# Kernel tuning notes

Measured on AMD Instinct MI355X. Metric: run time of the kernel, lower is better.

Reference implementation:

```python
import jax, jax.numpy as jnp
import numpy as np

B, N, M, D = 4096, 50, 64, 64   # batch, fields_dim, embedding_dim, product_layer_dim
V = 100000                      # features_dim (vocab)
HIDDEN = [512, 256, 128]
BN_EPS = 1e-3


def setup_inputs() -> dict:
    key = jax.random.key(0)
    ks = jax.random.split(key, 32)
    inp = {
        "feature_value": jax.random.uniform(ks[0], (B, N), dtype=jnp.float32),
        "embedding_index": jax.random.randint(ks[1], (B, N), 0, V, dtype=jnp.int32),
        "emb_table": jax.random.uniform(ks[2], (V, M), dtype=jnp.float32, minval=-0.05, maxval=0.05),
        "linear_signals": jax.random.normal(ks[3], (D, N, M), dtype=jnp.float32) * 0.05,
        "theta": jax.random.normal(ks[4], (D, N), dtype=jnp.float32) * 0.05,
        "quad_w": jax.random.normal(ks[5], (D, M, M), dtype=jnp.float32) * 0.05,
    }
    in_dim = 3 * D  # concat(l_z, l_p_inner, l_p_outer)
    dims = [in_dim] + HIDDEN
    k = 6
    for i, (di, do) in enumerate(zip(dims[:-1], dims[1:])):
        inp[f"W{i}"] = jax.random.normal(ks[k], (di, do), dtype=jnp.float32) * (1.0 / np.sqrt(di)); k += 1
        inp[f"b{i}"] = jnp.zeros((do,), dtype=jnp.float32)
        inp[f"g{i}"] = jnp.ones((do,), dtype=jnp.float32)
        inp[f"be{i}"] = jnp.zeros((do,), dtype=jnp.float32)
        inp[f"m{i}"] = jnp.zeros((do,), dtype=jnp.float32)
        inp[f"v{i}"] = jnp.ones((do,), dtype=jnp.float32)
    inp["Wout"] = jax.random.normal(ks[k], (HIDDEN[-1], 1), dtype=jnp.float32) * (1.0 / np.sqrt(HIDDEN[-1]))
    inp["bout"] = jnp.zeros((1,), dtype=jnp.float32)
    return inp


def _pnn_forward(feature_value, embedding_index, emb_table, linear_signals, theta, quad_w,
                 dense_params, Wout, bout):
    # features: [b, n, m] = embedding lookup scaled per-field by feature_value
    feats = emb_table[embedding_index] * feature_value[:, :, None]
    # linear signal: 'bnm,dnm->bd'
    l_z = jnp.einsum('bnm,dnm->bd', feats, linear_signals)
    # ipnn branch: delta = 'dn,bnm->bdnm'; l_p = sum delta*delta over (n,m)
    # algebraic rewrite (same math): sum_n theta_dn^2 * (sum_m feats_bnm^2)
    l_p_in = jnp.einsum('bn,dn->bd', jnp.sum(feats * feats, axis=2), theta * theta)
    # opnn branch: p = outer(sum_feats, sum_feats); 'bmn,dmn->bd'
    s = jnp.sum(feats, axis=1)  # [b, m]
    l_p_out = jnp.einsum('bm,dmn,bn->bd', s, quad_w, s)
    x = jnp.concatenate([l_z, l_p_in, l_p_out], axis=1)  # [b, 3d]
    # MLP stack: Dense -> BatchNorm(inference) -> ReLU (dropout is identity at eval)
    for (W, b, g, be, mu, var) in dense_params:
        x = x @ W + b
        x = g * (x - mu) * jax.lax.rsqrt(var + BN_EPS) + be
        x = jax.nn.relu(x)
    return jax.nn.sigmoid(x @ Wout + bout)


def reference(feature_value, embedding_index, emb_table, linear_signals, theta, quad_w,
              W0, b0, g0, be0, m0, v0,
              W1, b1, g1, be1, m1, v1,
              W2, b2, g2, be2, m2, v2,
              Wout, bout):
    dense_params = [(W0, b0, g0, be0, m0, v0),
                    (W1, b1, g1, be1, m1, v1),
                    (W2, b2, g2, be2, m2, v2)]
    return _pnn_forward(feature_value, embedding_index, emb_table, linear_signals, theta,
                        quad_w, dense_params, Wout, bout)
```

## Files before the change

### kernel.cpp

```cpp
#include <hip/hip_runtime.h>
#include <hip/hip_bf16.h>
#include <math.h>

#define B 4096
#define NF 50
#define BN_EPS 1e-3f
#define ROWS 16

typedef float f32x4 __attribute__((ext_vector_type(4)));
typedef __bf16 bf16x8 __attribute__((ext_vector_type(8)));
#define MFMA __builtin_amdgcn_mfma_f32_16x16x32_bf16

__device__ __forceinline__ unsigned short f2b(float x) {
  unsigned u = __float_as_uint(x);
  return (unsigned short)((u + 0x7FFFu + ((u >> 16) & 1u)) >> 16);
}
__device__ __forceinline__ unsigned packbf(float a, float b) {
  return ((unsigned)f2b(b) << 16) | (unsigned)f2b(a);
}
__device__ __forceinline__ float bs2f(unsigned short u) {
  return __uint_as_float(((unsigned)u) << 16);
}

#define WS_LS  0
#define WS_QW  204800
#define WS_W0  466944
#define WS_W1  565248
#define WS_W2  696320

__global__ __launch_bounds__(256) void prep(
    const float* __restrict__ ls, const float* __restrict__ qw,
    const float* __restrict__ W0, const float* __restrict__ W1,
    const float* __restrict__ W2, unsigned short* __restrict__ ws)
{
  int bid = blockIdx.x, t = threadIdx.x;
  if (bid < 228) {
    int o = (bid * 256 + t) * 8;
    const float* src = (o < 204800) ? (ls + o) : (qw + (o - 204800));
    float4 a = *(const float4*)src, b = *(const float4*)(src + 4);
    int4 v = {(int)packbf(a.x, a.y), (int)packbf(a.z, a.w),
              (int)packbf(b.x, b.y), (int)packbf(b.z, b.w)};
    *(int4*)&ws[o] = v;
    return;
  }
  __shared__ unsigned short sh[64 * 72];
  int id = bid - 228;
  const float* W; int K, Ncols, kt, nt, wofs;
  if (id < 24)      { W = W0; K = 192; Ncols = 512; kt = id >> 3; nt = id & 7;  wofs = WS_W0; }
  else if (id < 56) { int j = id - 24; W = W1; K = 512; Ncols = 256; kt = j >> 2; nt = j & 3; wofs = WS_W1; }
  else              { int j = id - 56; W = W2; K = 256; Ncols = 128; kt = j >> 1; nt = j & 1; wofs = WS_W2; }
  int k0 = kt * 64, n0 = nt * 64;
  {
    int r = t >> 2, cs = (t & 3) * 16;
    const float* src = W + (size_t)(k0 + r) * Ncols + n0 + cs;
    float4 a = *(const float4*)src, b = *(const float4*)(src + 4);
    float4 c = *(const float4*)(src + 8), d = *(const float4*)(src + 12);
    unsigned short* dst = &sh[r * 72 + cs];
    *(int4*)dst = int4{(int)packbf(a.x, a.y), (int)packbf(a.z, a.w),
                       (int)packbf(b.x, b.y), (int)packbf(b.z, b.w)};
    *(int4*)(dst + 8) = int4{(int)packbf(c.x, c.y), (int)packbf(c.z, c.w),
                             (int)packbf(d.x, d.y), (int)packbf(d.z, d.w)};
  }
  __syncthreads();
  {
    int nr = t >> 2, ks = (t & 3) * 16;
    unsigned short vbuf[16];
#pragma unroll
    for (int j = 0; j < 16; ++j) vbuf[j] = sh[(ks + j) * 72 + nr];
    unsigned short* dst = &ws[wofs + (size_t)(n0 + nr) * K + k0 + ks];
    *(int4*)dst = *(int4*)&vbuf[0];
    *(int4*)(dst + 8) = *(int4*)&vbuf[8];
  }
}

__global__ __launch_bounds__(512) void pnn_main(
    const float* __restrict__ fv, const int* __restrict__ idx,
    const float* __restrict__ emb, const float* __restrict__ theta,
    const unsigned short* __restrict__ ws,
    const float* __restrict__ b0p, const float* __restrict__ g0p,
    const float* __restrict__ be0p, const float* __restrict__ m0p,
    const float* __restrict__ v0p,
    const float* __restrict__ b1p, const float* __restrict__ g1p,
    const float* __restrict__ be1p, const float* __restrict__ m1p,
    const float* __restrict__ v1p,
    const float* __restrict__ b2p, const float* __restrict__ g2p,
    const float* __restrict__ be2p, const float* __restrict__ m2p,
    const float* __restrict__ v2p,
    const float* __restrict__ Wout, const float* __restrict__ boutp,
    float* __restrict__ out)
{
  __shared__ unsigned short feats[25 * 16 * 136];
  __shared__ int   idx_s[ROWS * NF];
  __shared__ float fv_s[ROWS * NF];
  __shared__ float s_s[ROWS * 68];
  __shared__ float sq_s[ROWS * 64];
  __shared__ unsigned short x_s[ROWS * 200];

  unsigned short* h0_s = feats;
  unsigned short* h1_s = feats + 8320;
  unsigned short* h2_s = feats + 12544;

  const unsigned short* lsb = ws + WS_LS;
  const unsigned short* qwb = ws + WS_QW;
  const unsigned short* w0t = ws + WS_W0;
  const unsigned short* w1t = ws + WS_W1;
  const unsigned short* w2t = ws + WS_W2;

  const int t    = threadIdx.x;
  const int w    = t >> 6;
  const int l    = t & 63;
  const int m16  = l & 15;
  const int qoff = (l >> 4) * 8;
  const int b0   = blockIdx.x * ROWS;

  for (int i = t; i < ROWS * NF; i += 512) {
    idx_s[i] = idx[b0 * NF + i];
    fv_s[i]  = fv[b0 * NF + i];
  }
  __syncthreads();

  {
    const int row = t >> 5;
    const int m2  = (t & 31) * 2;
    float s0 = 0.f, s1 = 0.f;
#pragma unroll 5
    for (int c = 0; c < 25; ++c) {
      int n0 = 2 * c, n1 = n0 + 1;
      int iv0 = idx_s[row * NF + n0], iv1 = idx_s[row * NF + n1];
      float f0 = fv_s[row * NF + n0], f1 = fv_s[row * NF + n1];
      float2 e0 = *(const float2*)(emb + (size_t)iv0 * 64 + m2);
      float2 e1 = *(const float2*)(emb + (size_t)iv1 * 64 + m2);
      float p00 = f0 * e0.x, p01 = f0 * e0.y;
      float p10 = f1 * e1.x, p11 = f1 * e1.y;
      unsigned short* fc = feats + c * 2176 + row * 136;
      *(unsigned*)&fc[m2]      = packbf(p00, p01);
      *(unsigned*)&fc[64 + m2] = packbf(p10, p11);
      s0 += p00 + p10; s1 += p01 + p11;
      float q0 = p00 * p00 + p01 * p01;
      float q1 = p10 * p10 + p11 * p11;
      q0 += __shfl_xor(q0, 16); q0 += __shfl_xor(q0, 8); q0 += __shfl_xor(q0, 4);
      q0 += __shfl_xor(q0, 2);  q0 += __shfl_xor(q0, 1);
      q1 += __shfl_xor(q1, 16); q1 += __shfl_xor(q1, 8); q1 += __shfl_xor(q1, 4);
      q1 += __shfl_xor(q1, 2);  q1 += __shfl_xor(q1, 1);
      if ((t & 31) == 0) { sq_s[row * 64 + n0] = q0; sq_s[row * 64 + n1] = q1; }
    }
    float2 sv; sv.x = s0; sv.y = s1;
    *(float2*)&s_s[row * 68 + m2] = sv;
  }
  __syncthreads();

  if (w < 4) {
    const int dt = w;
    f32x4 a0v = {0.f, 0.f, 0.f, 0.f}, a1v = {0.f, 0.f, 0.f, 0.f};
    const unsigned short* lp0 = lsb + (size_t)(dt * 16 + m16) * 3200 + qoff;
    for (int c = 0; c < 25; ++c) {
      const unsigned short* fc = feats + c * 2176 + m16 * 136 + qoff;
      const unsigned short* lp = lp0 + c * 128;
#pragma unroll
      for (int s = 0; s < 4; ++s) {
        bf16x8 av = *(const bf16x8*)(fc + s * 32);
        bf16x8 bv = *(const bf16x8*)(lp + s * 32);
        if (s & 1) a1v = MFMA(av, bv, a1v, 0, 0, 0);
        else       a0v = MFMA(av, bv, a0v, 0, 0, 0);
      }
    }
#pragma unroll
    for (int r = 0; r < 4; ++r)
      x_s[((l >> 4) * 4 + r) * 200 + dt * 16 + m16] = f2b(a0v[r] + a1v[r]);
    {
      int d = dt * 16 + m16;
      float acc[4] = {0.f, 0.f, 0.f, 0.f};
      for (int n = 0; n < NF; ++n) {
        float th = theta[d * NF + n];
        float th2 = th * th;
#pragma unroll
        for (int r = 0; r < 4; ++r)
          acc[r] += sq_s[((l >> 4) * 4 + r) * 64 + n] * th2;
      }
#pragma unroll
      for (int r = 0; r < 4; ++r)
        x_s[((l >> 4) * 4 + r) * 200 + 64 + d] = f2b(acc[r]);
    }
  } else {
    const int dt = w - 4;
    const int row = m16;
    const int nb = qoff;
    float sn[16];
    *(float4*)&sn[0]  = *(const float4*)&s_s[row * 68 + nb];
    *(float4*)&sn[4]  = *(const float4*)&s_s[row * 68 + nb + 4];
    *(float4*)&sn[8]  = *(const float4*)&s_s[row * 68 + 32 + nb];
    *(float4*)&sn[12] = *(const float4*)&s_s[row * 68 + 32 + nb + 4];
    f32x4 a0v = {0.f, 0.f, 0.f, 0.f}, a1v = {0.f, 0.f, 0.f, 0.f};
    const unsigned short* qp0 = qwb + (size_t)(dt * 16 + m16) * 4096 + qoff;
    for (int m = 0; m < 64; ++m) {
      float sm = s_s[row * 68 + m];
      union { unsigned u[4]; bf16x8 v; } af0, af1;
#pragma unroll
      for (int j = 0; j < 4; ++j) {
        af0.u[j] = packbf(sm * sn[2 * j],     sm * sn[2 * j + 1]);
        af1.u[j] = packbf(sm * sn[8 + 2 * j], sm * sn[8 + 2 * j + 1]);
      }
      const unsigned short* qp = qp0 + m * 64;
      bf16x8 b0v = *(const bf16x8*)qp;
      bf16x8 b1v = *(const bf16x8*)(qp + 32);
      a0v = MFMA(af0.v, b0v, a0v, 0, 0, 0);
      a1v = MFMA(af1.v, b1v, a1v, 0, 0, 0);
    }
#pragma unroll
    for (int r = 0; r < 4; ++r)
      x_s[((l >> 4) * 4 + r) * 200 + 128 + dt * 16 + m16] = f2b(a0v[r] + a1v[r]);
  }
  __syncthreads();

  {
    int ar = m16 * 200 + qoff;
    bf16x8 xa[6];
#pragma unroll
    for (int kc = 0; kc < 6; ++kc) xa[kc] = *(const bf16x8*)&x_s[ar + kc * 32];
    for (int j = 0; j < 4; ++j) {
      int n0 = (w * 4 + j) * 16;
      const unsigned short* wp = w0t + (size_t)(n0 + m16) * 192 + qoff;
      f32x4 ha = {0.f, 0.f, 0.f, 0.f}, hb = {0.f, 0.f, 0.f, 0.f};
#pragma unroll
      for (int kc = 0; kc < 6; ++kc) {
        bf16x8 bv = *(const bf16x8*)(wp + kc * 32);
        if (kc & 1) hb = MFMA(xa[kc], bv, hb, 0, 0, 0);
        else        ha = MFMA(xa[kc], bv, ha, 0, 0, 0);
      }
      int n = n0 + m16;
      float sc = g0p[n] * rsqrtf(v0p[n] + BN_EPS);
      float sh = be0p[n] + (b0p[n] - m0p[n]) * sc;
#pragma unroll
      for (int r = 0; r < 4; ++r) {
        float v = fmaxf((ha[r] + hb[r]) * sc + sh, 0.f);
        h0_s[((l >> 4) * 4 + r) * 520 + n] = f2b(v);
      }
    }
  }
  __syncthreads();

  for (int j = 0; j < 2; ++j) {
    int n0 = (w * 2 + j) * 16;
    const unsigned short* wp = w1t + (size_t)(n0 + m16) * 512 + qoff;
    int ar = m16 * 520 + qoff;
    f32x4 ha = {0.f, 0.f, 0.f, 0.f}, hb = {0.f, 0.f, 0.f, 0.f};
#pragma unroll
    for (int kc = 0; kc < 16; ++kc) {
      bf16x8 av = *(const bf16x8*)&h0_s[ar + kc * 32];
      bf16x8 bv = *(const bf16x8*)(wp + kc * 32);
      if (kc & 1) hb = MFMA(av, bv, hb, 0, 0, 0);
      else        ha = MFMA(av, bv, ha, 0, 0, 0);
    }
    int n = n0 + m16;
    float sc = g1p[n] * rsqrtf(v1p[n] + BN_EPS);
    float sh = be1p[n] + (b1p[n] - m1p[n]) * sc;
#pragma unroll
    for (int r = 0; r < 4; ++r) {
      float v = fmaxf((ha[r] + hb[r]) * sc + sh, 0.f);
      h1_s[((l >> 4) * 4 + r) * 264 + n] = f2b(v);
    }
  }
  __syncthreads();

  {
    int n0 = w * 16;
    const unsigned short* wp = w2t + (size_t)(n0 + m16) * 256 + qoff;
    int ar = m16 * 264 + qoff;
    f32x4 ha = {0.f, 0.f, 0.f, 0.f}, hb = {0.f, 0.f, 0.f, 0.f};
#pragma unroll
    for (int kc = 0; kc < 8; ++kc) {
      bf16x8 av = *(const bf16x8*)&h1_s[ar + kc * 32];
      bf16x8 bv = *(const bf16x8*)(wp + kc * 32);
      if (kc & 1) hb = MFMA(av, bv, hb, 0, 0, 0);
      else        ha = MFMA(av, bv, ha, 0, 0, 0);
    }
    int n = n0 + m16;
    float sc = g2p[n] * rsqrtf(v2p[n] + BN_EPS);
    float sh = be2p[n] + (b2p[n] - m2p[n]) * sc;
#pragma unroll
    for (int r = 0; r < 4; ++r) {
      float v = fmaxf((ha[r] + hb[r]) * sc + sh, 0.f);
      h2_s[((l >> 4) * 4 + r) * 136 + n] = f2b(v);
    }
  }
  __syncthreads();

  if (t < 128) {
    int bb = t >> 3, seg = t & 7;
    float a = 0.f;
#pragma unroll
    for (int j = 0; j < 16; ++j) {
      int k = seg * 16 + j;
      a += bs2f(h2_s[bb * 136 + k]) * Wout[k];
    }
    a += __shfl_xor(a, 4); a += __shfl_xor(a, 2); a += __shfl_xor(a, 1);
    if (seg == 0) out[b0 + bb] = 1.f / (1.f + expf(-(a + boutp[0])));
  }
}

extern "C" void kernel_launch(void* const* d_in, const int* in_sizes, int n_in,
                              void* d_out, int out_size, void* d_ws, size_t ws_size,
                              hipStream_t stream)
{
  (void)in_sizes; (void)n_in; (void)out_size; (void)ws_size;
  unsigned short* ws = (unsigned short*)d_ws;

  prep<<<292, 256, 0, stream>>>(
      (const float*)d_in[3], (const float*)d_in[5], (const float*)d_in[6],
      (const float*)d_in[12], (const float*)d_in[18], ws);

  pnn_main<<<B / ROWS, 512, 0, stream>>>(
      (const float*)d_in[0], (const int*)d_in[1], (const float*)d_in[2],
      (const float*)d_in[4], ws,
      (const float*)d_in[7],  (const float*)d_in[8],  (const float*)d_in[9],
      (const float*)d_in[10], (const float*)d_in[11],
      (const float*)d_in[13], (const float*)d_in[14], (const float*)d_in[15],
      (const float*)d_in[16], (const float*)d_in[17],
      (const float*)d_in[19], (const float*)d_in[20], (const float*)d_in[21],
      (const float*)d_in[22], (const float*)d_in[23],
      (const float*)d_in[24], (const float*)d_in[25],
      (float*)d_out);
}
```

Baseline: 182.2 us.

## Drop weight prep kernel and convert fp32 weights to bf16 inside main kernel

Removes the separate prep launch that pre-converted linear_signals, quad_w and the MLP weights to bf16, with the MLP weights also transposed. The main kernel now reads the fp32 weights directly and packs them to bf16 in registers, using strided scalar loads for the untransposed MLP weights. This saves one launch and the workspace round trip. In exchange, each of the 256 blocks re-reads twice the weight bytes and does its own conversion, and the MLP weight reads become strided, uncoalesced scalar loads.

```diff
diff --git a/kernel.cpp b/kernel.cpp
--- a/kernel.cpp
+++ b/kernel.cpp
@@ -21,71 +21,36 @@
 __device__ __forceinline__ float bs2f(unsigned short u) {
   return __uint_as_float(((unsigned)u) << 16);
 }
-
-#define WS_LS  0
-#define WS_QW  204800
-#define WS_W0  466944
-#define WS_W1  565248
-#define WS_W2  696320
-
-__global__ __launch_bounds__(256) void prep(
-    const float* __restrict__ ls, const float* __restrict__ qw,
-    const float* __restrict__ W0, const float* __restrict__ W1,
-    const float* __restrict__ W2, unsigned short* __restrict__ ws)
-{
-  int bid = blockIdx.x, t = threadIdx.x;
-  if (bid < 228) {
-    int o = (bid * 256 + t) * 8;
-    const float* src = (o < 204800) ? (ls + o) : (qw + (o - 204800));
-    float4 a = *(const float4*)src, b = *(const float4*)(src + 4);
-    int4 v = {(int)packbf(a.x, a.y), (int)packbf(a.z, a.w),
-              (int)packbf(b.x, b.y), (int)packbf(b.z, b.w)};
-    *(int4*)&ws[o] = v;
-    return;
-  }
-  __shared__ unsigned short sh[64 * 72];
-  int id = bid - 228;
-  const float* W; int K, Ncols, kt, nt, wofs;
-  if (id < 24)      { W = W0; K = 192; Ncols = 512; kt = id >> 3; nt = id & 7;  wofs = WS_W0; }
-  else if (id < 56) { int j = id - 24; W = W1; K = 512; Ncols = 256; kt = j >> 2; nt = j & 3; wofs = WS_W1; }
-  else              { int j = id - 56; W = W2; K = 256; Ncols = 128; kt = j >> 1; nt = j & 1; wofs = WS_W2; }
-  int k0 = kt * 64, n0 = nt * 64;
-  {
-    int r = t >> 2, cs = (t & 3) * 16;
-    const float* src = W + (size_t)(k0 + r) * Ncols + n0 + cs;
-    float4 a = *(const float4*)src, b = *(const float4*)(src + 4);
-    float4 c = *(const float4*)(src + 8), d = *(const float4*)(src + 12);
-    unsigned short* dst = &sh[r * 72 + cs];
-    *(int4*)dst = int4{(int)packbf(a.x, a.y), (int)packbf(a.z, a.w),
-                       (int)packbf(b.x, b.y), (int)packbf(b.z, b.w)};
-    *(int4*)(dst + 8) = int4{(int)packbf(c.x, c.y), (int)packbf(c.z, c.w),
-                             (int)packbf(d.x, d.y), (int)packbf(d.z, d.w)};
-  }
-  __syncthreads();
-  {
-    int nr = t >> 2, ks = (t & 3) * 16;
-    unsigned short vbuf[16];
-#pragma unroll
-    for (int j = 0; j < 16; ++j) vbuf[j] = sh[(ks + j) * 72 + nr];
-    unsigned short* dst = &ws[wofs + (size_t)(n0 + nr) * K + k0 + ks];
-    *(int4*)dst = *(int4*)&vbuf[0];
-    *(int4*)(dst + 8) = *(int4*)&vbuf[8];
-  }
-}
-
-__global__ __launch_bounds__(512) void pnn_main(
+__device__ __forceinline__ bf16x8 ld_bf8(const float* p) {
+  float4 a = *(const float4*)p, b = *(const float4*)(p + 4);
+  union { unsigned u[4]; bf16x8 v; } r;
+  r.u[0] = packbf(a.x, a.y); r.u[1] = packbf(a.z, a.w);
+  r.u[2] = packbf(b.x, b.y); r.u[3] = packbf(b.z, b.w);
+  return r.v;
+}
+__device__ __forceinline__ bf16x8 ld_bf8_strided(const float* p, int stride) {
+  float f[8];
+#pragma unroll
+  for (int j = 0; j < 8; ++j) f[j] = p[j * stride];
+  union { unsigned u[4]; bf16x8 v; } r;
+  r.u[0] = packbf(f[0], f[1]); r.u[1] = packbf(f[2], f[3]);
+  r.u[2] = packbf(f[4], f[5]); r.u[3] = packbf(f[6], f[7]);
+  return r.v;
+}
+
+__global__ __launch_bounds__(512) void pnn_all(
     const float* __restrict__ fv, const int* __restrict__ idx,
     const float* __restrict__ emb, const float* __restrict__ theta,
-    const unsigned short* __restrict__ ws,
-    const float* __restrict__ b0p, const float* __restrict__ g0p,
-    const float* __restrict__ be0p, const float* __restrict__ m0p,
-    const float* __restrict__ v0p,
-    const float* __restrict__ b1p, const float* __restrict__ g1p,
-    const float* __restrict__ be1p, const float* __restrict__ m1p,
-    const float* __restrict__ v1p,
-    const float* __restrict__ b2p, const float* __restrict__ g2p,
-    const float* __restrict__ be2p, const float* __restrict__ m2p,
-    const float* __restrict__ v2p,
+    const float* __restrict__ ls, const float* __restrict__ qw,
+    const float* __restrict__ W0, const float* __restrict__ b0p,
+    const float* __restrict__ g0p, const float* __restrict__ be0p,
+    const float* __restrict__ m0p, const float* __restrict__ v0p,
+    const float* __restrict__ W1, const float* __restrict__ b1p,
+    const float* __restrict__ g1p, const float* __restrict__ be1p,
+    const float* __restrict__ m1p, const float* __restrict__ v1p,
+    const float* __restrict__ W2, const float* __restrict__ b2p,
+    const float* __restrict__ g2p, const float* __restrict__ be2p,
+    const float* __restrict__ m2p, const float* __restrict__ v2p,
     const float* __restrict__ Wout, const float* __restrict__ boutp,
     float* __restrict__ out)
 {
@@ -99,12 +64,6 @@
   unsigned short* h0_s = feats;
   unsigned short* h1_s = feats + 8320;
   unsigned short* h2_s = feats + 12544;
-
-  const unsigned short* lsb = ws + WS_LS;
-  const unsigned short* qwb = ws + WS_QW;
-  const unsigned short* w0t = ws + WS_W0;
-  const unsigned short* w1t = ws + WS_W1;
-  const unsigned short* w2t = ws + WS_W2;
 
   const int t    = threadIdx.x;
   const int w    = t >> 6;
@@ -152,14 +111,14 @@
   if (w < 4) {
     const int dt = w;
     f32x4 a0v = {0.f, 0.f, 0.f, 0.f}, a1v = {0.f, 0.f, 0.f, 0.f};
-    const unsigned short* lp0 = lsb + (size_t)(dt * 16 + m16) * 3200 + qoff;
+    const float* lp0 = ls + (size_t)(dt * 16 + m16) * 3200 + qoff;
     for (int c = 0; c < 25; ++c) {
       const unsigned short* fc = feats + c * 2176 + m16 * 136 + qoff;
-      const unsigned short* lp = lp0 + c * 128;
+      const float* lp = lp0 + c * 128;
 #pragma unroll
       for (int s = 0; s < 4; ++s) {
         bf16x8 av = *(const bf16x8*)(fc + s * 32);
-        bf16x8 bv = *(const bf16x8*)(lp + s * 32);
+        bf16x8 bv = ld_bf8(lp + s * 32);
         if (s & 1) a1v = MFMA(av, bv, a1v, 0, 0, 0);
         else       a0v = MFMA(av, bv, a0v, 0, 0, 0);
       }
@@ -191,7 +150,7 @@
     *(float4*)&sn[8]  = *(const float4*)&s_s[row * 68 + 32 + nb];
     *(float4*)&sn[12] = *(const float4*)&s_s[row * 68 + 32 + nb + 4];
     f32x4 a0v = {0.f, 0.f, 0.f, 0.f}, a1v = {0.f, 0.f, 0.f, 0.f};
-    const unsigned short* qp0 = qwb + (size_t)(dt * 16 + m16) * 4096 + qoff;
+    const float* qp0 = qw + (size_t)(dt * 16 + m16) * 4096 + qoff;
     for (int m = 0; m < 64; ++m) {
       float sm = s_s[row * 68 + m];
       union { unsigned u[4]; bf16x8 v; } af0, af1;
@@ -200,9 +159,9 @@
         af0.u[j] = packbf(sm * sn[2 * j],     sm * sn[2 * j + 1]);
         af1.u[j] = packbf(sm * sn[8 + 2 * j], sm * sn[8 + 2 * j + 1]);
       }
-      const unsigned short* qp = qp0 + m * 64;
-      bf16x8 b0v = *(const bf16x8*)qp;
-      bf16x8 b1v = *(const bf16x8*)(qp + 32);
+      const float* qp = qp0 + m * 64;
+      bf16x8 b0v = ld_bf8(qp);
+      bf16x8 b1v = ld_bf8(qp + 32);
       a0v = MFMA(af0.v, b0v, a0v, 0, 0, 0);
       a1v = MFMA(af1.v, b1v, a1v, 0, 0, 0);
     }
@@ -219,11 +178,10 @@
     for (int kc = 0; kc < 6; ++kc) xa[kc] = *(const bf16x8*)&x_s[ar + kc * 32];
     for (int j = 0; j < 4; ++j) {
       int n0 = (w * 4 + j) * 16;
-      const unsigned short* wp = w0t + (size_t)(n0 + m16) * 192 + qoff;
       f32x4 ha = {0.f, 0.f, 0.f, 0.f}, hb = {0.f, 0.f, 0.f, 0.f};
 #pragma unroll
       for (int kc = 0; kc < 6; ++kc) {
-        bf16x8 bv = *(const bf16x8*)(wp + kc * 32);
+        bf16x8 bv = ld_bf8_strided(W0 + (size_t)(kc * 32 + qoff) * 512 + n0 + m16, 512);
         if (kc & 1) hb = MFMA(xa[kc], bv, hb, 0, 0, 0);
         else        ha = MFMA(xa[kc], bv, ha, 0, 0, 0);
       }
@@ -241,13 +199,12 @@
 
   for (int j = 0; j < 2; ++j) {
     int n0 = (w * 2 + j) * 16;
-    const unsigned short* wp = w1t + (size_t)(n0 + m16) * 512 + qoff;
     int ar = m16 * 520 + qoff;
     f32x4 ha = {0.f, 0.f, 0.f, 0.f}, hb = {0.f, 0.f, 0.f, 0.f};
 #pragma unroll
     for (int kc = 0; kc < 16; ++kc) {
       bf16x8 av = *(const bf16x8*)&h0_s[ar + kc * 32];
-      bf16x8 bv = *(const bf16x8*)(wp + kc * 32);
+      bf16x8 bv = ld_bf8_strided(W1 + (size_t)(kc * 32 + qoff) * 256 + n0 + m16, 256);
       if (kc & 1) hb = MFMA(av, bv, hb, 0, 0, 0);
       else        ha = MFMA(av, bv, ha, 0, 0, 0);
     }
@@ -264,13 +221,12 @@
 
   {
     int n0 = w * 16;
-    const unsigned short* wp = w2t + (size_t)(n0 + m16) * 256 + qoff;
     int ar = m16 * 264 + qoff;
     f32x4 ha = {0.f, 0.f, 0.f, 0.f}, hb = {0.f, 0.f, 0.f, 0.f};
 #pragma unroll
     for (int kc = 0; kc < 8; ++kc) {
       bf16x8 av = *(const bf16x8*)&h1_s[ar + kc * 32];
-      bf16x8 bv = *(const bf16x8*)(wp + kc * 32);
+      bf16x8 bv = ld_bf8_strided(W2 + (size_t)(kc * 32 + qoff) * 128 + n0 + m16, 128);
       if (kc & 1) hb = MFMA(av, bv, hb, 0, 0, 0);
       else        ha = MFMA(av, bv, ha, 0, 0, 0);
     }
@@ -302,22 +258,17 @@
                               void* d_out, int out_size, void* d_ws, size_t ws_size,
                               hipStream_t stream)
 {
-  (void)in_sizes; (void)n_in; (void)out_size; (void)ws_size;
-  unsigned short* ws = (unsigned short*)d_ws;
-
-  prep<<<292, 256, 0, stream>>>(
-      (const float*)d_in[3], (const float*)d_in[5], (const float*)d_in[6],
-      (const float*)d_in[12], (const float*)d_in[18], ws);
-
-  pnn_main<<<B / ROWS, 512, 0, stream>>>(
+  (void)in_sizes; (void)n_in; (void)out_size; (void)d_ws; (void)ws_size;
+
+  pnn_all<<<B / ROWS, 512, 0, stream>>>(
       (const float*)d_in[0], (const int*)d_in[1], (const float*)d_in[2],
-      (const float*)d_in[4], ws,
-      (const float*)d_in[7],  (const float*)d_in[8],  (const float*)d_in[9],
-      (const float*)d_in[10], (const float*)d_in[11],
-      (const float*)d_in[13], (const float*)d_in[14], (const float*)d_in[15],
-      (const float*)d_in[16], (const float*)d_in[17],
-      (const float*)d_in[19], (const float*)d_in[20], (const float*)d_in[21],
-      (const float*)d_in[22], (const float*)d_in[23],
+      (const float*)d_in[4], (const float*)d_in[3], (const float*)d_in[5],
+      (const float*)d_in[6],  (const float*)d_in[7],  (const float*)d_in[8],
+      (const float*)d_in[9],  (const float*)d_in[10], (const float*)d_in[11],
+      (const float*)d_in[12], (const float*)d_in[13], (const float*)d_in[14],
+      (const float*)d_in[15], (const float*)d_in[16], (const float*)d_in[17],
+      (const float*)d_in[18], (const float*)d_in[19], (const float*)d_in[20],
+      (const float*)d_in[21], (const float*)d_in[22], (const float*)d_in[23],
       (const float*)d_in[24], (const float*)d_in[25],
       (float*)d_out);
 }
```

Result: slower. 245.0 us (+34.4%).

## Halve rows per block to 8 and remap gather, MFMA rows and theta staging

Applied to the files above, without the earlier changes.

Cuts the rows per block from 16 to 8, which doubles the grid to 512 blocks and shrinks shared memory. The launch-bounds minimum of 4 blocks per SM is meant to raise occupancy. The embedding gather is remapped to one wave per row with coalesced scalar loads, and theta squared is staged in shared memory instead of being re-read from global. MFMA tiles still compute 16 rows, so half the matrix work is duplicated and half the lanes are masked on stores, and every block now reloads all weights.

```diff
diff --git a/kernel.cpp b/kernel.cpp
--- a/kernel.cpp
+++ b/kernel.cpp
@@ -5,7 +5,7 @@
 #define B 4096
 #define NF 50
 #define BN_EPS 1e-3f
-#define ROWS 16
+#define ROWS 8
 
 typedef float f32x4 __attribute__((ext_vector_type(4)));
 typedef __bf16 bf16x8 __attribute__((ext_vector_type(8)));
@@ -73,7 +73,7 @@
   }
 }
 
-__global__ __launch_bounds__(512) void pnn_main(
+__global__ __launch_bounds__(512, 4) void pnn_main(
     const float* __restrict__ fv, const int* __restrict__ idx,
     const float* __restrict__ emb, const float* __restrict__ theta,
     const unsigned short* __restrict__ ws,
@@ -89,16 +89,17 @@
     const float* __restrict__ Wout, const float* __restrict__ boutp,
     float* __restrict__ out)
 {
-  __shared__ unsigned short feats[25 * 16 * 136];
+  __shared__ unsigned short feats[25 * ROWS * 136];
   __shared__ int   idx_s[ROWS * NF];
   __shared__ float fv_s[ROWS * NF];
+  __shared__ float th2_s[64 * NF];
   __shared__ float s_s[ROWS * 68];
   __shared__ float sq_s[ROWS * 64];
   __shared__ unsigned short x_s[ROWS * 200];
 
   unsigned short* h0_s = feats;
-  unsigned short* h1_s = feats + 8320;
-  unsigned short* h2_s = feats + 12544;
+  unsigned short* h1_s = feats + 4160;
+  unsigned short* h2_s = feats + 6272;
 
   const unsigned short* lsb = ws + WS_LS;
   const unsigned short* qwb = ws + WS_QW;
@@ -117,35 +118,24 @@
     idx_s[i] = idx[b0 * NF + i];
     fv_s[i]  = fv[b0 * NF + i];
   }
-  __syncthreads();
-
-  {
-    const int row = t >> 5;
-    const int m2  = (t & 31) * 2;
-    float s0 = 0.f, s1 = 0.f;
-#pragma unroll 5
-    for (int c = 0; c < 25; ++c) {
-      int n0 = 2 * c, n1 = n0 + 1;
-      int iv0 = idx_s[row * NF + n0], iv1 = idx_s[row * NF + n1];
-      float f0 = fv_s[row * NF + n0], f1 = fv_s[row * NF + n1];
-      float2 e0 = *(const float2*)(emb + (size_t)iv0 * 64 + m2);
-      float2 e1 = *(const float2*)(emb + (size_t)iv1 * 64 + m2);
-      float p00 = f0 * e0.x, p01 = f0 * e0.y;
-      float p10 = f1 * e1.x, p11 = f1 * e1.y;
-      unsigned short* fc = feats + c * 2176 + row * 136;
-      *(unsigned*)&fc[m2]      = packbf(p00, p01);
-      *(unsigned*)&fc[64 + m2] = packbf(p10, p11);
-      s0 += p00 + p10; s1 += p01 + p11;
-      float q0 = p00 * p00 + p01 * p01;
-      float q1 = p10 * p10 + p11 * p11;
-      q0 += __shfl_xor(q0, 16); q0 += __shfl_xor(q0, 8); q0 += __shfl_xor(q0, 4);
-      q0 += __shfl_xor(q0, 2);  q0 += __shfl_xor(q0, 1);
-      q1 += __shfl_xor(q1, 16); q1 += __shfl_xor(q1, 8); q1 += __shfl_xor(q1, 4);
-      q1 += __shfl_xor(q1, 2);  q1 += __shfl_xor(q1, 1);
-      if ((t & 31) == 0) { sq_s[row * 64 + n0] = q0; sq_s[row * 64 + n1] = q1; }
-    }
-    float2 sv; sv.x = s0; sv.y = s1;
-    *(float2*)&s_s[row * 68 + m2] = sv;
+  for (int i = t; i < 64 * NF; i += 512) { float v = theta[i]; th2_s[i] = v * v; }
+  __syncthreads();
+
+  {
+    float s0 = 0.f;
+#pragma unroll 2
+    for (int n = 0; n < NF; ++n) {
+      int iv = idx_s[w * NF + n];
+      float fvv = fv_s[w * NF + n];
+      float p = fvv * emb[(size_t)iv * 64 + l];
+      feats[(n >> 1) * (ROWS * 136) + w * 136 + (n & 1) * 64 + l] = f2b(p);
+      s0 += p;
+      float q = p * p;
+      q += __shfl_xor(q, 32); q += __shfl_xor(q, 16); q += __shfl_xor(q, 8);
+      q += __shfl_xor(q, 4);  q += __shfl_xor(q, 2);  q += __shfl_xor(q, 1);
+      if (l == 0) sq_s[w * 64 + n] = q;
+    }
+    s_s[w * 68 + l] = s0;
   }
   __syncthreads();
 
@@ -153,8 +143,9 @@
     const int dt = w;
     f32x4 a0v = {0.f, 0.f, 0.f, 0.f}, a1v = {0.f, 0.f, 0.f, 0.f};
     const unsigned short* lp0 = lsb + (size_t)(dt * 16 + m16) * 3200 + qoff;
+    const int arow = (m16 & 7) * 136 + qoff;
     for (int c = 0; c < 25; ++c) {
-      const unsigned short* fc = feats + c * 2176 + m16 * 136 + qoff;
+      const unsigned short* fc = feats + c * (ROWS * 136) + arow;
       const unsigned short* lp = lp0 + c * 128;
 #pragma unroll
       for (int s = 0; s < 4; ++s) {
@@ -164,15 +155,16 @@
         else       a0v = MFMA(av, bv, a0v, 0, 0, 0);
       }
     }
-#pragma unroll
-    for (int r = 0; r < 4; ++r)
-      x_s[((l >> 4) * 4 + r) * 200 + dt * 16 + m16] = f2b(a0v[r] + a1v[r]);
-    {
+    if (l < 32) {
+#pragma unroll
+      for (int r = 0; r < 4; ++r)
+        x_s[((l >> 4) * 4 + r) * 200 + dt * 16 + m16] = f2b(a0v[r] + a1v[r]);
+    }
+    if (l < 32) {
       int d = dt * 16 + m16;
       float acc[4] = {0.f, 0.f, 0.f, 0.f};
       for (int n = 0; n < NF; ++n) {
-        float th = theta[d * NF + n];
-        float th2 = th * th;
+        float th2 = th2_s[d * NF + n];
 #pragma unroll
         for (int r = 0; r < 4; ++r)
           acc[r] += sq_s[((l >> 4) * 4 + r) * 64 + n] * th2;
@@ -183,7 +175,7 @@
     }
   } else {
     const int dt = w - 4;
-    const int row = m16;
+    const int row = m16 & 7;
     const int nb = qoff;
     float sn[16];
     *(float4*)&sn[0]  = *(const float4*)&s_s[row * 68 + nb];
@@ -206,14 +198,16 @@
       a0v = MFMA(af0.v, b0v, a0v, 0, 0, 0);
       a1v = MFMA(af1.v, b1v, a1v, 0, 0, 0);
     }
-#pragma unroll
-    for (int r = 0; r < 4; ++r)
-      x_s[((l >> 4) * 4 + r) * 200 + 128 + dt * 16 + m16] = f2b(a0v[r] + a1v[r]);
-  }
-  __syncthreads();
-
-  {
-    int ar = m16 * 200 + qoff;
+    if (l < 32) {
+#pragma unroll
+      for (int r = 0; r < 4; ++r)
+        x_s[((l >> 4) * 4 + r) * 200 + 128 + dt * 16 + m16] = f2b(a0v[r] + a1v[r]);
+    }
+  }
+  __syncthreads();
+
+  {
+    int ar = (m16 & 7) * 200 + qoff;
     bf16x8 xa[6];
 #pragma unroll
     for (int kc = 0; kc < 6; ++kc) xa[kc] = *(const bf16x8*)&x_s[ar + kc * 32];
@@ -227,13 +221,15 @@
         if (kc & 1) hb = MFMA(xa[kc], bv, hb, 0, 0, 0);
         else        ha = MFMA(xa[kc], bv, ha, 0, 0, 0);
       }
-      int n = n0 + m16;
-      float sc = g0p[n] * rsqrtf(v0p[n] + BN_EPS);
-      float sh = be0p[n] + (b0p[n] - m0p[n]) * sc;
-#pragma unroll
-      for (int r = 0; r < 4; ++r) {
-        float v = fmaxf((ha[r] + hb[r]) * sc + sh, 0.f);
-        h0_s[((l >> 4) * 4 + r) * 520 + n] = f2b(v);
+      if (l < 32) {
+        int n = n0 + m16;
+        float sc = g0p[n] * rsqrtf(v0p[n] + BN_EPS);
+        float sh = be0p[n] + (b0p[n] - m0p[n]) * sc;
+#pragma unroll
+        for (int r = 0; r < 4; ++r) {
+          float v = fmaxf((ha[r] + hb[r]) * sc + sh, 0.f);
+          h0_s[((l >> 4) * 4 + r) * 520 + n] = f2b(v);
+        }
       }
     }
   }
@@ -242,7 +238,7 @@
   for (int j = 0; j < 2; ++j) {
     int n0 = (w * 2 + j) * 16;
     const unsigned short* wp = w1t + (size_t)(n0 + m16) * 512 + qoff;
-    int ar = m16 * 520 + qoff;
+    int ar = (m16 & 7) * 520 + qoff;
     f32x4 ha = {0.f, 0.f, 0.f, 0.f}, hb = {0.f, 0.f, 0.f, 0.f};
 #pragma unroll
     for (int kc = 0; kc < 16; ++kc) {
@@ -251,13 +247,15 @@
       if (kc & 1) hb = MFMA(av, bv, hb, 0, 0, 0);
       else        ha = MFMA(av, bv, ha, 0, 0, 0);
     }
-    int n = n0 + m16;
-    float sc = g1p[n] * rsqrtf(v1p[n] + BN_EPS);
-    float sh = be1p[n] + (b1p[n] - m1p[n]) * sc;
-#pragma unroll
-    for (int r = 0; r < 4; ++r) {
-      float v = fmaxf((ha[r] + hb[r]) * sc + sh, 0.f);
-      h1_s[((l >> 4) * 4 + r) * 264 + n] = f2b(v);
+    if (l < 32) {
+      int n = n0 + m16;
+      float sc = g1p[n] * rsqrtf(v1p[n] + BN_EPS);
+      float sh = be1p[n] + (b1p[n] - m1p[n]) * sc;
+#pragma unroll
+      for (int r = 0; r < 4; ++r) {
+        float v = fmaxf((ha[r] + hb[r]) * sc + sh, 0.f);
+        h1_s[((l >> 4) * 4 + r) * 264 + n] = f2b(v);
+      }
     }
   }
   __syncthreads();
@@ -265,7 +263,7 @@
   {
     int n0 = w * 16;
     const unsigned short* wp = w2t + (size_t)(n0 + m16) * 256 + qoff;
-    int ar = m16 * 264 + qoff;
+    int ar = (m16 & 7) * 264 + qoff;
     f32x4 ha = {0.f, 0.f, 0.f, 0.f}, hb = {0.f, 0.f, 0.f, 0.f};
 #pragma unroll
     for (int kc = 0; kc < 8; ++kc) {
@@ -274,18 +272,20 @@
       if (kc & 1) hb = MFMA(av, bv, hb, 0, 0, 0);
       else        ha = MFMA(av, bv, ha, 0, 0, 0);
     }
-    int n = n0 + m16;
-    float sc = g2p[n] * rsqrtf(v2p[n] + BN_EPS);
-    float sh = be2p[n] + (b2p[n] - m2p[n]) * sc;
-#pragma unroll
-    for (int r = 0; r < 4; ++r) {
-      float v = fmaxf((ha[r] + hb[r]) * sc + sh, 0.f);
-      h2_s[((l >> 4) * 4 + r) * 136 + n] = f2b(v);
-    }
-  }
-  __syncthreads();
-
-  if (t < 128) {
+    if (l < 32) {
+      int n = n0 + m16;
+      float sc = g2p[n] * rsqrtf(v2p[n] + BN_EPS);
+      float sh = be2p[n] + (b2p[n] - m2p[n]) * sc;
+#pragma unroll
+      for (int r = 0; r < 4; ++r) {
+        float v = fmaxf((ha[r] + hb[r]) * sc + sh, 0.f);
+        h2_s[((l >> 4) * 4 + r) * 136 + n] = f2b(v);
+      }
+    }
+  }
+  __syncthreads();
+
+  if (t < 64) {
     int bb = t >> 3, seg = t & 7;
     float a = 0.f;
 #pragma unroll
```

Result: slower. 228.6 us (+25.4%).

## Batch global loads ahead of MFMA chains and cache squared theta in LDS

Applied to the files above, without the earlier changes.

Restructures the embedding gather, linear-signal, quadratic and MLP loops so that groups of global loads (embedding rows, bf16 weight fragments) are issued into register arrays before the dependent MFMA or arithmetic runs. The goal is more memory-level parallelism and better hiding of global-load latency. It also precomputes theta squared into shared memory once per block, so the ipnn loop no longer does per-lane global loads and squares. The cost is higher register pressure, which may lower occupancy, plus extra LDS and a per-block theta load.

```diff
diff --git a/kernel.cpp b/kernel.cpp
--- a/kernel.cpp
+++ b/kernel.cpp
@@ -92,6 +92,7 @@
   __shared__ unsigned short feats[25 * 16 * 136];
   __shared__ int   idx_s[ROWS * NF];
   __shared__ float fv_s[ROWS * NF];
+  __shared__ float th2_s[64 * NF];
   __shared__ float s_s[ROWS * 68];
   __shared__ float sq_s[ROWS * 64];
   __shared__ unsigned short x_s[ROWS * 200];
@@ -117,32 +118,41 @@
     idx_s[i] = idx[b0 * NF + i];
     fv_s[i]  = fv[b0 * NF + i];
   }
+  for (int i = t; i < 64 * NF; i += 512) { float v = theta[i]; th2_s[i] = v * v; }
   __syncthreads();
 
   {
     const int row = t >> 5;
     const int m2  = (t & 31) * 2;
     float s0 = 0.f, s1 = 0.f;
-#pragma unroll 5
-    for (int c = 0; c < 25; ++c) {
-      int n0 = 2 * c, n1 = n0 + 1;
-      int iv0 = idx_s[row * NF + n0], iv1 = idx_s[row * NF + n1];
-      float f0 = fv_s[row * NF + n0], f1 = fv_s[row * NF + n1];
-      float2 e0 = *(const float2*)(emb + (size_t)iv0 * 64 + m2);
-      float2 e1 = *(const float2*)(emb + (size_t)iv1 * 64 + m2);
-      float p00 = f0 * e0.x, p01 = f0 * e0.y;
-      float p10 = f1 * e1.x, p11 = f1 * e1.y;
-      unsigned short* fc = feats + c * 2176 + row * 136;
-      *(unsigned*)&fc[m2]      = packbf(p00, p01);
-      *(unsigned*)&fc[64 + m2] = packbf(p10, p11);
-      s0 += p00 + p10; s1 += p01 + p11;
-      float q0 = p00 * p00 + p01 * p01;
-      float q1 = p10 * p10 + p11 * p11;
-      q0 += __shfl_xor(q0, 16); q0 += __shfl_xor(q0, 8); q0 += __shfl_xor(q0, 4);
-      q0 += __shfl_xor(q0, 2);  q0 += __shfl_xor(q0, 1);
-      q1 += __shfl_xor(q1, 16); q1 += __shfl_xor(q1, 8); q1 += __shfl_xor(q1, 4);
-      q1 += __shfl_xor(q1, 2);  q1 += __shfl_xor(q1, 1);
-      if ((t & 31) == 0) { sq_s[row * 64 + n0] = q0; sq_s[row * 64 + n1] = q1; }
+    for (int g = 0; g < 5; ++g) {
+      float2 e[10];
+#pragma unroll
+      for (int j = 0; j < 5; ++j) {
+        int n0 = (g * 5 + j) * 2;
+        int iv0 = idx_s[row * NF + n0], iv1 = idx_s[row * NF + n0 + 1];
+        e[2 * j]     = *(const float2*)(emb + (size_t)iv0 * 64 + m2);
+        e[2 * j + 1] = *(const float2*)(emb + (size_t)iv1 * 64 + m2);
+      }
+#pragma unroll
+      for (int j = 0; j < 5; ++j) {
+        int c = g * 5 + j;
+        int n0 = 2 * c, n1 = n0 + 1;
+        float f0 = fv_s[row * NF + n0], f1 = fv_s[row * NF + n1];
+        float p00 = f0 * e[2 * j].x,     p01 = f0 * e[2 * j].y;
+        float p10 = f1 * e[2 * j + 1].x, p11 = f1 * e[2 * j + 1].y;
+        unsigned short* fc = feats + c * 2176 + row * 136;
+        *(unsigned*)&fc[m2]      = packbf(p00, p01);
+        *(unsigned*)&fc[64 + m2] = packbf(p10, p11);
+        s0 += p00 + p10; s1 += p01 + p11;
+        float q0 = p00 * p00 + p01 * p01;
+        float q1 = p10 * p10 + p11 * p11;
+        q0 += __shfl_xor(q0, 16); q0 += __shfl_xor(q0, 8); q0 += __shfl_xor(q0, 4);
+        q0 += __shfl_xor(q0, 2);  q0 += __shfl_xor(q0, 1);
+        q1 += __shfl_xor(q1, 16); q1 += __shfl_xor(q1, 8); q1 += __shfl_xor(q1, 4);
+        q1 += __shfl_xor(q1, 2);  q1 += __shfl_xor(q1, 1);
+        if ((t & 31) == 0) { sq_s[row * 64 + n0] = q0; sq_s[row * 64 + n1] = q1; }
+      }
     }
     float2 sv; sv.x = s0; sv.y = s1;
     *(float2*)&s_s[row * 68 + m2] = sv;
@@ -153,15 +163,25 @@
     const int dt = w;
     f32x4 a0v = {0.f, 0.f, 0.f, 0.f}, a1v = {0.f, 0.f, 0.f, 0.f};
     const unsigned short* lp0 = lsb + (size_t)(dt * 16 + m16) * 3200 + qoff;
-    for (int c = 0; c < 25; ++c) {
-      const unsigned short* fc = feats + c * 2176 + m16 * 136 + qoff;
-      const unsigned short* lp = lp0 + c * 128;
-#pragma unroll
-      for (int s = 0; s < 4; ++s) {
-        bf16x8 av = *(const bf16x8*)(fc + s * 32);
-        bf16x8 bv = *(const bf16x8*)(lp + s * 32);
-        if (s & 1) a1v = MFMA(av, bv, a1v, 0, 0, 0);
-        else       a0v = MFMA(av, bv, a0v, 0, 0, 0);
+    const int arow = m16 * 136 + qoff;
+    for (int g = 0; g < 5; ++g) {
+      bf16x8 bv[20];
+#pragma unroll
+      for (int cc = 0; cc < 5; ++cc) {
+        const unsigned short* lp = lp0 + (g * 5 + cc) * 128;
+#pragma unroll
+        for (int s4 = 0; s4 < 4; ++s4)
+          bv[cc * 4 + s4] = *(const bf16x8*)(lp + s4 * 32);
+      }
+#pragma unroll
+      for (int cc = 0; cc < 5; ++cc) {
+        const unsigned short* fc = feats + (g * 5 + cc) * 2176 + arow;
+#pragma unroll
+        for (int s4 = 0; s4 < 4; ++s4) {
+          bf16x8 av = *(const bf16x8*)(fc + s4 * 32);
+          if (s4 & 1) a1v = MFMA(av, bv[cc * 4 + s4], a1v, 0, 0, 0);
+          else        a0v = MFMA(av, bv[cc * 4 + s4], a0v, 0, 0, 0);
+        }
       }
     }
 #pragma unroll
@@ -171,8 +191,7 @@
       int d = dt * 16 + m16;
       float acc[4] = {0.f, 0.f, 0.f, 0.f};
       for (int n = 0; n < NF; ++n) {
-        float th = theta[d * NF + n];
-        float th2 = th * th;
+        float th2 = th2_s[d * NF + n];
 #pragma unroll
         for (int r = 0; r < 4; ++r)
           acc[r] += sq_s[((l >> 4) * 4 + r) * 64 + n] * th2;
@@ -192,19 +211,26 @@
     *(float4*)&sn[12] = *(const float4*)&s_s[row * 68 + 32 + nb + 4];
     f32x4 a0v = {0.f, 0.f, 0.f, 0.f}, a1v = {0.f, 0.f, 0.f, 0.f};
     const unsigned short* qp0 = qwb + (size_t)(dt * 16 + m16) * 4096 + qoff;
-    for (int m = 0; m < 64; ++m) {
-      float sm = s_s[row * 68 + m];
-      union { unsigned u[4]; bf16x8 v; } af0, af1;
-#pragma unroll
-      for (int j = 0; j < 4; ++j) {
-        af0.u[j] = packbf(sm * sn[2 * j],     sm * sn[2 * j + 1]);
-        af1.u[j] = packbf(sm * sn[8 + 2 * j], sm * sn[8 + 2 * j + 1]);
-      }
-      const unsigned short* qp = qp0 + m * 64;
-      bf16x8 b0v = *(const bf16x8*)qp;
-      bf16x8 b1v = *(const bf16x8*)(qp + 32);
-      a0v = MFMA(af0.v, b0v, a0v, 0, 0, 0);
-      a1v = MFMA(af1.v, b1v, a1v, 0, 0, 0);
+    for (int g = 0; g < 8; ++g) {
+      bf16x8 bv[16];
+#pragma unroll
+      for (int mi = 0; mi < 8; ++mi) {
+        const unsigned short* qp = qp0 + (g * 8 + mi) * 64;
+        bv[2 * mi]     = *(const bf16x8*)qp;
+        bv[2 * mi + 1] = *(const bf16x8*)(qp + 32);
+      }
+#pragma unroll
+      for (int mi = 0; mi < 8; ++mi) {
+        float sm = s_s[row * 68 + g * 8 + mi];
+        union { unsigned u[4]; bf16x8 v; } af0, af1;
+#pragma unroll
+        for (int j = 0; j < 4; ++j) {
+          af0.u[j] = packbf(sm * sn[2 * j],     sm * sn[2 * j + 1]);
+          af1.u[j] = packbf(sm * sn[8 + 2 * j], sm * sn[8 + 2 * j + 1]);
+        }
+        a0v = MFMA(af0.v, bv[2 * mi],     a0v, 0, 0, 0);
+        a1v = MFMA(af1.v, bv[2 * mi + 1], a1v, 0, 0, 0);
+      }
     }
 #pragma unroll
     for (int r = 0; r < 4; ++r)
@@ -220,12 +246,14 @@
     for (int j = 0; j < 4; ++j) {
       int n0 = (w * 4 + j) * 16;
       const unsigned short* wp = w0t + (size_t)(n0 + m16) * 192 + qoff;
+      bf16x8 bv[6];
+#pragma unroll
+      for (int kc = 0; kc < 6; ++kc) bv[kc] = *(const bf16x8*)(wp + kc * 32);
       f32x4 ha = {0.f, 0.f, 0.f, 0.f}, hb = {0.f, 0.f, 0.f, 0.f};
 #pragma unroll
       for (int kc = 0; kc < 6; ++kc) {
-        bf16x8 bv = *(const bf16x8*)(wp + kc * 32);
-        if (kc & 1) hb = MFMA(xa[kc], bv, hb, 0, 0, 0);
-        else        ha = MFMA(xa[kc], bv, ha, 0, 0, 0);
+        if (kc & 1) hb = MFMA(xa[kc], bv[kc], hb, 0, 0, 0);
+        else        ha = MFMA(xa[kc], bv[kc], ha, 0, 0, 0);
       }
       int n = n0 + m16;
       float sc = g0p[n] * rsqrtf(v0p[n] + BN_EPS);
@@ -242,14 +270,16 @@
   for (int j = 0; j < 2; ++j) {
     int n0 = (w * 2 + j) * 16;
     const unsigned short* wp = w1t + (size_t)(n0 + m16) * 512 + qoff;
+    bf16x8 bv[16];
+#pragma unroll
+    for (int kc = 0; kc < 16; ++kc) bv[kc] = *(const bf16x8*)(wp + kc * 32);
     int ar = m16 * 520 + qoff;
     f32x4 ha = {0.f, 0.f, 0.f, 0.f}, hb = {0.f, 0.f, 0.f, 0.f};
 #pragma unroll
     for (int kc = 0; kc < 16; ++kc) {
       bf16x8 av = *(const bf16x8*)&h0_s[ar + kc * 32];
-      bf16x8 bv = *(const bf16x8*)(wp + kc * 32);
-      if (kc & 1) hb = MFMA(av, bv, hb, 0, 0, 0);
-      else        ha = MFMA(av, bv, ha, 0, 0, 0);
+      if (kc & 1) hb = MFMA(av, bv[kc], hb, 0, 0, 0);
+      else        ha = MFMA(av, bv[kc], ha, 0, 0, 0);
     }
     int n = n0 + m16;
     float sc = g1p[n] * rsqrtf(v1p[n] + BN_EPS);
@@ -265,14 +295,16 @@
   {
     int n0 = w * 16;
     const unsigned short* wp = w2t + (size_t)(n0 + m16) * 256 + qoff;
+    bf16x8 bv[8];
+#pragma unroll
+    for (int kc = 0; kc < 8; ++kc) bv[kc] = *(const bf16x8*)(wp + kc * 32);
     int ar = m16 * 264 + qoff;
     f32x4 ha = {0.f, 0.f, 0.f, 0.f}, hb = {0.f, 0.f, 0.f, 0.f};
 #pragma unroll
     for (int kc = 0; kc < 8; ++kc) {
       bf16x8 av = *(const bf16x8*)&h1_s[ar + kc * 32];
-      bf16x8 bv = *(const bf16x8*)(wp + kc * 32);
-      if (kc & 1) hb = MFMA(av, bv, hb, 0, 0, 0);
-      else        ha = MFMA(av, bv, ha, 0, 0, 0);
+      if (kc & 1) hb = MFMA(av, bv[kc], hb, 0, 0, 0);
+      else        ha = MFMA(av, bv[kc], ha, 0, 0, 0);
     }
     int n = n0 + m16;
     float sc = g2p[n] * rsqrtf(v2p[n] + BN_EPS);
```

Measured after the change: 172.6 us. 5.3% less time.
